# Kernel optimization log

Hardware: AMD Instinct MI355X
Metric: run time of the kernel (lower is better)

The kernel has to match this reference:

```python
import jax, jax.numpy as jnp
import numpy as np

NIN, DIM, NHEAD = 512, 64, 8
B, N = 2, 2048

def setup_inputs() -> dict:
    key = jax.random.key(0)
    ks = jax.random.split(key, 7)
    s = 1.0 / np.sqrt(NIN)  # torch Linear default init range
    out_f = DIM * NHEAD
    return {
        "x": jax.random.normal(ks[0], (B, N, NIN), dtype=jnp.float32),
        "Wq": jax.random.uniform(ks[1], (out_f, NIN), jnp.float32, -s, s),
        "bq": jax.random.uniform(ks[2], (out_f,), jnp.float32, -s, s),
        "Wk": jax.random.uniform(ks[3], (out_f, NIN), jnp.float32, -s, s),
        "bk": jax.random.uniform(ks[4], (out_f,), jnp.float32, -s, s),
        "Wv": jax.random.uniform(ks[5], (out_f, NIN), jnp.float32, -s, s),
        "bv": jax.random.uniform(ks[6], (out_f,), jnp.float32, -s, s),
    }

def reference(x, Wq, bq, Wk, bk, Wv, bv):
    b, n, nin = x.shape
    scale = DIM ** (-0.5)
    # torch: self.qs(x).view(nhead, B, N, dim) -- a FLAT reshape, not a transpose
    q = (x @ Wq.T + bq).reshape(NHEAD, b, n, DIM)
    k = (x @ Wk.T + bk).reshape(NHEAD, b, n, DIM)
    v = (x @ Wv.T + bv).reshape(NHEAD, b, n, DIM)
    # no softmax in the original module; mask path is a no-op (masked_fill not in-place)
    att = jnp.einsum('hbid,hbjd->hbij', q, k) * scale  # [h,b,n,n]
    out = jnp.einsum('hbij,hbjd->hbid', att, v)        # [h,b,n,d]
    out = jnp.transpose(out, (1, 2, 3, 0))             # [b,n,d,h]
    return out.reshape(b, n, -1)
```

## Files before the change

### kernel.cpp

```cpp
#include <hip/hip_runtime.h>
#include <stdint.h>

#define CHELEM 131072

typedef __attribute__((ext_vector_type(4))) float   f32x4;
typedef __attribute__((ext_vector_type(8))) short   bh8;
typedef __attribute__((ext_vector_type(4))) unsigned short u16x4;
typedef __attribute__((ext_vector_type(8))) unsigned short u16x8;
typedef unsigned short u16;

__device__ inline u16 f2bf(float f) {
    union { float f; uint32_t u; } v; v.f = f;
    uint32_t u = v.u;
    u += 0x7FFF + ((u >> 16) & 1);
    return (u16)(u >> 16);
}

__device__ inline void gload_lds16(const u16* g, u16* l) {
    __builtin_amdgcn_global_load_lds(
        (const __attribute__((address_space(1))) uint32_t*)g,
        (__attribute__((address_space(3)))       uint32_t*)l,
        16, 0, 0);
}

__global__ __launch_bounds__(256) void k0_convert(
        const float* __restrict__ x,
        const float* __restrict__ Wq,
        const float* __restrict__ Wk,
        const float* __restrict__ Wv,
        u16* __restrict__ xb, u16* __restrict__ Wb) {
    int idx = blockIdx.x * 256 + threadIdx.x;
    const float4* src; u16* dst; int off;
    if (idx < 524288) { src = (const float4*)x; dst = xb; off = idx; }
    else {
        int j = idx - 524288;
        int w = j >> 16;
        off = j & 65535;
        src = (const float4*)(w == 0 ? Wq : (w == 1 ? Wk : Wv));
        dst = Wb + w * 262144;
    }
    float4 f = src[off];
    u16x4 o;
    o[0] = f2bf(f.x); o[1] = f2bf(f.y); o[2] = f2bf(f.z); o[3] = f2bf(f.w);
    *(u16x4*)(dst + off * 4) = o;
}

__global__ __launch_bounds__(256) void k1_qkv(
        const u16* __restrict__ xb, const u16* __restrict__ Wb,
        const float* __restrict__ bq, const float* __restrict__ bk,
        const float* __restrict__ bv,
        u16* __restrict__ Qb, u16* __restrict__ Kb, u16* __restrict__ Vb) {
    __shared__ u16 smem[12288];
    u16* lA = smem;
    u16* lB = smem + 4096;
    const int tid  = threadIdx.x;
    const int lane = tid & 63, wid = tid >> 6;
    const int wr = wid >> 1, wc = wid & 1;
    const int swz  = (blockIdx.x & 7) * 96 + (blockIdx.x >> 3);
    const int mb = swz / 12, nb = swz % 12;
    const int w    = nb >> 2;
    const int nloc = (nb & 3) * 128;
    const u16*   W    = Wb + w * 262144;
    const float* bias = (w == 0) ? bq : ((w == 1) ? bk : bv);
    u16*         out  = (w == 0) ? Qb : ((w == 1) ? Kb : Vb);
    const int m0 = mb * 64;

    f32x4 acc[2][4] = {};
    const int srow = tid >> 3;
    const int scol = (tid & 7) * 8;

    for (int kb = 0; kb < 8; ++kb) {
        __syncthreads();
        const int k0 = kb * 64;
#pragma unroll
        for (int it = 0; it < 2; ++it) {
            int r = it * 32 + srow;
            gload_lds16(xb + (size_t)(m0 + r) * 512 + k0 + scol, lA + r * 64 + scol);
        }
#pragma unroll
        for (int it = 0; it < 4; ++it) {
            int r = it * 32 + srow;
            gload_lds16(W + (size_t)(nloc + r) * 512 + k0 + scol, lB + r * 64 + scol);
        }
        asm volatile("s_waitcnt vmcnt(0)" ::: "memory");
        __syncthreads();
#pragma unroll
        for (int ks = 0; ks < 2; ++ks) {
            const int kk = ks * 32 + (lane >> 4) * 8;
            bh8 a[2], b[4];
#pragma unroll
            for (int i = 0; i < 2; ++i)
                a[i] = *(const bh8*)&lA[(wr * 32 + i * 16 + (lane & 15)) * 64 + kk];
#pragma unroll
            for (int j = 0; j < 4; ++j)
                b[j] = *(const bh8*)&lB[(wc * 64 + j * 16 + (lane & 15)) * 64 + kk];
#pragma unroll
            for (int i = 0; i < 2; ++i)
#pragma unroll
                for (int j = 0; j < 4; ++j)
                    acc[i][j] = __builtin_amdgcn_mfma_f32_16x16x32_bf16(a[i], b[j], acc[i][j], 0, 0, 0);
        }
    }

    if (w == 0) {
#pragma unroll
        for (int i = 0; i < 2; ++i) {
            const int row_base = m0 + wr * 32 + i * 16 + ((lane >> 4) * 4);
#pragma unroll
            for (int j = 0; j < 4; ++j) {
                const int col = nloc + wc * 64 + j * 16 + (lane & 15);
                const float bv_ = bias[col];
#pragma unroll
                for (int r = 0; r < 4; ++r)
                    out[(size_t)(row_base + r) * 512 + col] = f2bf(acc[i][j][r] + bv_);
            }
        }
    } else {
        __syncthreads();
        u16 (*tile)[130] = (u16(*)[130])smem;
#pragma unroll
        for (int i = 0; i < 2; ++i) {
            const int ml = wr * 32 + i * 16 + ((lane >> 4) * 4);
#pragma unroll
            for (int j = 0; j < 4; ++j) {
                const int nl = wc * 64 + j * 16 + (lane & 15);
                const float bv_ = bias[nloc + nl];
#pragma unroll
                for (int r = 0; r < 4; ++r)
                    tile[ml + r][nl] = f2bf(acc[i][j][r] + bv_);
            }
        }
        __syncthreads();
        const int ncol  = tid & 127;
        const int mhalf = tid >> 7;
        const int g = (nb & 3) * 2 + (ncol >> 6);
        const int d = ncol & 63;
        const int c = mb >> 2;
        const int qbase = (mb & 3) * 64 + mhalf * 32;
        u16* dst = out + (size_t)c * CHELEM + d * 2048 + g * 256 + qbase;
#pragma unroll
        for (int v = 0; v < 4; ++v) {
            u16x8 t;
#pragma unroll
            for (int j = 0; j < 8; ++j)
                t[j] = tile[mhalf * 32 + v * 8 + j][ncol];
            *(u16x8*)(dst + v * 8) = t;
        }
    }
}

__global__ __launch_bounds__(256) void k2_pmat(
        const u16* __restrict__ Kt2, const u16* __restrict__ Vt2,
        u16* __restrict__ Pb) {
    __shared__ float red[4][16][16];
    const int tid = threadIdx.x;
    const int lane = tid & 63, w = tid >> 6;
    const int c   = blockIdx.x & 15;
    const int sub = blockIdx.x >> 4;
    const int dq = sub >> 2, eq = sub & 3;
    const u16* Vc = Vt2 + (size_t)c * CHELEM;
    const u16* Kc = Kt2 + (size_t)c * CHELEM;
    const int krow = lane & 15;
    const int arow = (dq * 16 + krow) * 2048;
    const int brow = (eq * 16 + krow) * 2048;
    const int kb = w * 512 + (lane >> 4) * 8;

    f32x4 acc = {};
#pragma unroll
    for (int kt = 0; kt < 16; ++kt) {
        const int k0 = kb + kt * 32;
        bh8 a = *(const bh8*)&Vc[arow + k0];
        bh8 b = *(const bh8*)&Kc[brow + k0];
        acc = __builtin_amdgcn_mfma_f32_16x16x32_bf16(a, b, acc, 0, 0, 0);
    }
#pragma unroll
    for (int r = 0; r < 4; ++r)
        red[w][(lane >> 4) * 4 + r][lane & 15] = acc[r];
    __syncthreads();
    const int row = tid >> 4, col = tid & 15;
    float s = red[0][row][col] + red[1][row][col] + red[2][row][col] + red[3][row][col];
    Pb[c * 4096 + (dq * 16 + row) * 64 + eq * 16 + col] = f2bf(s * 0.125f);
}

__global__ __launch_bounds__(256) void k3_out(
        const u16* __restrict__ Qb, const u16* __restrict__ Pb,
        float* __restrict__ outp) {
    const int tid = threadIdx.x;
    const int lane = tid & 63, w = tid >> 6;
    const int bb = blockIdx.x >> 6;
    const int ib = blockIdx.x & 63;
    const int i0 = ib * 32 + (w >> 1) * 16;
    const int dbase = (w & 1) * 32;
    const int krow = lane & 15;
    const int koff = (lane >> 4) * 8;

    f32x4 acc[8][2] = {};
#pragma unroll
    for (int h = 0; h < 8; ++h) {
        const int c = h * 2 + bb;
        const u16* Qc = Qb + (size_t)c * CHELEM;
        const u16* Pc = Pb + c * 4096;
#pragma unroll
        for (int ks = 0; ks < 2; ++ks) {
            bh8 a = *(const bh8*)&Qc[(i0 + krow) * 64 + ks * 32 + koff];
#pragma unroll
            for (int nf = 0; nf < 2; ++nf) {
                bh8 b = *(const bh8*)&Pc[(dbase + nf * 16 + krow) * 64 + ks * 32 + koff];
                acc[h][nf] = __builtin_amdgcn_mfma_f32_16x16x32_bf16(a, b, acc[h][nf], 0, 0, 0);
            }
        }
    }
    const int orow_base = bb * 2048 + ib * 32 + (w >> 1) * 16 + (lane >> 4) * 4;
#pragma unroll
    for (int nf = 0; nf < 2; ++nf) {
        const int d = dbase + nf * 16 + (lane & 15);
#pragma unroll
        for (int r = 0; r < 4; ++r) {
            f32x4 lo = {acc[0][nf][r], acc[1][nf][r], acc[2][nf][r], acc[3][nf][r]};
            f32x4 hi = {acc[4][nf][r], acc[5][nf][r], acc[6][nf][r], acc[7][nf][r]};
            float* dst = outp + (size_t)(orow_base + r) * 512 + d * 8;
            *(f32x4*)dst = lo;
            *(f32x4*)(dst + 4) = hi;
        }
    }
}

extern "C" void kernel_launch(void* const* d_in, const int* in_sizes, int n_in,
                              void* d_out, int out_size, void* d_ws, size_t ws_size,
                              hipStream_t stream) {
    const float* x  = (const float*)d_in[0];
    const float* Wq = (const float*)d_in[1];
    const float* bq = (const float*)d_in[2];
    const float* Wk = (const float*)d_in[3];
    const float* bk = (const float*)d_in[4];
    const float* Wv = (const float*)d_in[5];
    const float* bv = (const float*)d_in[6];
    float* outp = (float*)d_out;

    u16* xb = (u16*)d_ws;
    u16* Wb = xb + 2097152;
    u16* Qb = Wb + 786432;
    u16* Kb = Qb + 2097152;
    u16* Vb = Kb + 2097152;
    u16* Pb = Vb + 2097152;

    k0_convert<<<2816, 256, 0, stream>>>(x, Wq, Wk, Wv, xb, Wb);
    k1_qkv<<<768, 256, 0, stream>>>(xb, Wb, bq, bk, bv, Qb, Kb, Vb);
    k2_pmat<<<256, 256, 0, stream>>>(Kb, Vb, Pb);
    k3_out<<<128, 256, 0, stream>>>(Qb, Pb, outp);
}
```

Measured before the change: 41.20 us.

## Fuse P-matrix and output kernels with a global atomic flag barrier

Merges k2_pmat and k3_out into one 128-block launch. The first 16 blocks each compute a full 64x64 P matrix per chunk, using a 4x4 MFMA tile per wave and an LDS reduction across waves, then signal completion with an atomic counter. All blocks spin on that counter before running the Q·P output stage. This removes one kernel launch and its gap, but it relies on all 128 blocks being co-resident and puts all P work on only 16 blocks, which serialises that stage. The spin wait has an iteration cap, so it could time out and read P before it is written.

```diff
diff --git a/kernel.cpp b/kernel.cpp
--- a/kernel.cpp
+++ b/kernel.cpp
@@ -28,7 +28,10 @@
         const float* __restrict__ Wq,
         const float* __restrict__ Wk,
         const float* __restrict__ Wv,
-        u16* __restrict__ xb, u16* __restrict__ Wb) {
+        u16* __restrict__ xb, u16* __restrict__ Wb,
+        int* __restrict__ flag) {
+    if (blockIdx.x == 0 && threadIdx.x == 0)
+        __hip_atomic_store(flag, 0, __ATOMIC_RELAXED, __HIP_MEMORY_SCOPE_AGENT);
     int idx = blockIdx.x * 256 + threadIdx.x;
     const float4* src; u16* dst; int off;
     if (idx < 524288) { src = (const float4*)x; dst = xb; off = idx; }
@@ -149,52 +152,76 @@
     }
 }
 
-__global__ __launch_bounds__(256) void k2_pmat(
+__global__ __launch_bounds__(256) void k23_pv(
         const u16* __restrict__ Kt2, const u16* __restrict__ Vt2,
-        u16* __restrict__ Pb) {
-    __shared__ float red[4][16][16];
+        const u16* __restrict__ Qb, u16* __restrict__ Pb,
+        int* __restrict__ flag, float* __restrict__ outp) {
+    __shared__ float red[4][4096];
     const int tid = threadIdx.x;
     const int lane = tid & 63, w = tid >> 6;
-    const int c   = blockIdx.x & 15;
-    const int sub = blockIdx.x >> 4;
-    const int dq = sub >> 2, eq = sub & 3;
-    const u16* Vc = Vt2 + (size_t)c * CHELEM;
-    const u16* Kc = Kt2 + (size_t)c * CHELEM;
-    const int krow = lane & 15;
-    const int arow = (dq * 16 + krow) * 2048;
-    const int brow = (eq * 16 + krow) * 2048;
-    const int kb = w * 512 + (lane >> 4) * 8;
-
-    f32x4 acc = {};
-#pragma unroll
-    for (int kt = 0; kt < 16; ++kt) {
-        const int k0 = kb + kt * 32;
-        bh8 a = *(const bh8*)&Vc[arow + k0];
-        bh8 b = *(const bh8*)&Kc[brow + k0];
-        acc = __builtin_amdgcn_mfma_f32_16x16x32_bf16(a, b, acc, 0, 0, 0);
-    }
-#pragma unroll
-    for (int r = 0; r < 4; ++r)
-        red[w][(lane >> 4) * 4 + r][lane & 15] = acc[r];
+    const int bid = blockIdx.x;
+
+    if (bid < 16) {
+        const int c = bid;
+        const u16* Ac = Vt2 + (size_t)c * CHELEM;
+        const u16* Bc = Kt2 + (size_t)c * CHELEM;
+        f32x4 acc[4][4] = {};
+        const int krow = lane & 15;
+        const int kbase = w * 512 + (lane >> 4) * 8;
+#pragma unroll 4
+        for (int kt = 0; kt < 16; ++kt) {
+            const int k0 = kbase + kt * 32;
+            bh8 a[4], b[4];
+#pragma unroll
+            for (int i = 0; i < 4; ++i) {
+                a[i] = *(const bh8*)&Ac[(i * 16 + krow) * 2048 + k0];
+                b[i] = *(const bh8*)&Bc[(i * 16 + krow) * 2048 + k0];
+            }
+#pragma unroll
+            for (int i = 0; i < 4; ++i)
+#pragma unroll
+                for (int j = 0; j < 4; ++j)
+                    acc[i][j] = __builtin_amdgcn_mfma_f32_16x16x32_bf16(a[i], b[j], acc[i][j], 0, 0, 0);
+        }
+#pragma unroll
+        for (int i = 0; i < 4; ++i)
+#pragma unroll
+            for (int j = 0; j < 4; ++j)
+#pragma unroll
+                for (int r = 0; r < 4; ++r)
+                    red[w][(i * 16 + (lane >> 4) * 4 + r) * 64 + j * 16 + (lane & 15)] = acc[i][j][r];
+        __syncthreads();
+        u16* Pc = Pb + c * 4096;
+#pragma unroll
+        for (int q = 0; q < 16; ++q) {
+            const int idx = q * 256 + tid;
+            float s = red[0][idx] + red[1][idx] + red[2][idx] + red[3][idx];
+            Pc[idx] = f2bf(s * 0.125f);
+        }
+        __syncthreads();
+        if (tid == 0) {
+            __threadfence();
+            __hip_atomic_fetch_add(flag, 1, __ATOMIC_RELEASE, __HIP_MEMORY_SCOPE_AGENT);
+        }
+    }
+
+    if (tid == 0) {
+        int it = 0;
+        while (__hip_atomic_load(flag, __ATOMIC_ACQUIRE, __HIP_MEMORY_SCOPE_AGENT) < 16) {
+            __builtin_amdgcn_s_sleep(8);
+            if (++it > 1000000) break;
+        }
+    }
     __syncthreads();
-    const int row = tid >> 4, col = tid & 15;
-    float s = red[0][row][col] + red[1][row][col] + red[2][row][col] + red[3][row][col];
-    Pb[c * 4096 + (dq * 16 + row) * 64 + eq * 16 + col] = f2bf(s * 0.125f);
-}
-
-__global__ __launch_bounds__(256) void k3_out(
-        const u16* __restrict__ Qb, const u16* __restrict__ Pb,
-        float* __restrict__ outp) {
-    const int tid = threadIdx.x;
-    const int lane = tid & 63, w = tid >> 6;
-    const int bb = blockIdx.x >> 6;
-    const int ib = blockIdx.x & 63;
+
+    const int bb = bid >> 6;
+    const int ib = bid & 63;
     const int i0 = ib * 32 + (w >> 1) * 16;
     const int dbase = (w & 1) * 32;
     const int krow = lane & 15;
     const int koff = (lane >> 4) * 8;
 
-    f32x4 acc[8][2] = {};
+    f32x4 acc2[8][2] = {};
 #pragma unroll
     for (int h = 0; h < 8; ++h) {
         const int c = h * 2 + bb;
@@ -206,7 +233,7 @@
 #pragma unroll
             for (int nf = 0; nf < 2; ++nf) {
                 bh8 b = *(const bh8*)&Pc[(dbase + nf * 16 + krow) * 64 + ks * 32 + koff];
-                acc[h][nf] = __builtin_amdgcn_mfma_f32_16x16x32_bf16(a, b, acc[h][nf], 0, 0, 0);
+                acc2[h][nf] = __builtin_amdgcn_mfma_f32_16x16x32_bf16(a, b, acc2[h][nf], 0, 0, 0);
             }
         }
     }
@@ -216,8 +243,8 @@
         const int d = dbase + nf * 16 + (lane & 15);
 #pragma unroll
         for (int r = 0; r < 4; ++r) {
-            f32x4 lo = {acc[0][nf][r], acc[1][nf][r], acc[2][nf][r], acc[3][nf][r]};
-            f32x4 hi = {acc[4][nf][r], acc[5][nf][r], acc[6][nf][r], acc[7][nf][r]};
+            f32x4 lo = {acc2[0][nf][r], acc2[1][nf][r], acc2[2][nf][r], acc2[3][nf][r]};
+            f32x4 hi = {acc2[4][nf][r], acc2[5][nf][r], acc2[6][nf][r], acc2[7][nf][r]};
             float* dst = outp + (size_t)(orow_base + r) * 512 + d * 8;
             *(f32x4*)dst = lo;
             *(f32x4*)(dst + 4) = hi;
@@ -243,9 +270,9 @@
     u16* Kb = Qb + 2097152;
     u16* Vb = Kb + 2097152;
     u16* Pb = Vb + 2097152;
-
-    k0_convert<<<2816, 256, 0, stream>>>(x, Wq, Wk, Wv, xb, Wb);
+    int* flag = (int*)(Pb + 65536);
+
+    k0_convert<<<2816, 256, 0, stream>>>(x, Wq, Wk, Wv, xb, Wb, flag);
     k1_qkv<<<768, 256, 0, stream>>>(xb, Wb, bq, bk, bv, Qb, Kb, Vb);
-    k2_pmat<<<256, 256, 0, stream>>>(Kb, Vb, Pb);
-    k3_out<<<128, 256, 0, stream>>>(Qb, Pb, outp);
-}
+    k23_pv<<<128, 256, 0, stream>>>(Kb, Vb, Qb, Pb, flag, outp);
+}
```

Result: slower. 86.19 us (+109.2%).

## Fuse P-matrix and output kernels with a device-wide atomic barrier

Applied to the files above, without the earlier changes.

Merges the K^T V reduction kernel and the Q·P output kernel into one launch. An atomic counter acts as a grid-wide barrier: each block publishes its P tile, then spins until all 256 blocks have finished before starting the output GEMM. The output phase is re-tiled so each of the 256 blocks handles a 16-row slice. This removes one kernel launch and its gap, at the cost of relying on all 256 blocks being co-resident, plus a spin-wait with a timeout that could silently yield wrong results if the timeout is hit.

```diff
diff --git a/kernel.cpp b/kernel.cpp
--- a/kernel.cpp
+++ b/kernel.cpp
@@ -28,7 +28,10 @@
         const float* __restrict__ Wq,
         const float* __restrict__ Wk,
         const float* __restrict__ Wv,
-        u16* __restrict__ xb, u16* __restrict__ Wb) {
+        u16* __restrict__ xb, u16* __restrict__ Wb,
+        int* __restrict__ flag) {
+    if (blockIdx.x == 0 && threadIdx.x == 0)
+        __hip_atomic_store(flag, 0, __ATOMIC_RELAXED, __HIP_MEMORY_SCOPE_AGENT);
     int idx = blockIdx.x * 256 + threadIdx.x;
     const float4* src; u16* dst; int off;
     if (idx < 524288) { src = (const float4*)x; dst = xb; off = idx; }
@@ -149,52 +152,64 @@
     }
 }
 
-__global__ __launch_bounds__(256) void k2_pmat(
+__global__ __launch_bounds__(256) void k23_pv(
         const u16* __restrict__ Kt2, const u16* __restrict__ Vt2,
-        u16* __restrict__ Pb) {
+        const u16* __restrict__ Qb, u16* __restrict__ Pb,
+        int* __restrict__ flag, float* __restrict__ outp) {
     __shared__ float red[4][16][16];
     const int tid = threadIdx.x;
     const int lane = tid & 63, w = tid >> 6;
-    const int c   = blockIdx.x & 15;
-    const int sub = blockIdx.x >> 4;
-    const int dq = sub >> 2, eq = sub & 3;
-    const u16* Vc = Vt2 + (size_t)c * CHELEM;
-    const u16* Kc = Kt2 + (size_t)c * CHELEM;
-    const int krow = lane & 15;
-    const int arow = (dq * 16 + krow) * 2048;
-    const int brow = (eq * 16 + krow) * 2048;
-    const int kb = w * 512 + (lane >> 4) * 8;
-
-    f32x4 acc = {};
-#pragma unroll
-    for (int kt = 0; kt < 16; ++kt) {
-        const int k0 = kb + kt * 32;
-        bh8 a = *(const bh8*)&Vc[arow + k0];
-        bh8 b = *(const bh8*)&Kc[brow + k0];
-        acc = __builtin_amdgcn_mfma_f32_16x16x32_bf16(a, b, acc, 0, 0, 0);
-    }
-#pragma unroll
-    for (int r = 0; r < 4; ++r)
-        red[w][(lane >> 4) * 4 + r][lane & 15] = acc[r];
+    const int bid = blockIdx.x;
+
+    {
+        const int c   = bid & 15;
+        const int sub = bid >> 4;
+        const int dq = sub >> 2, eq = sub & 3;
+        const u16* Vc = Vt2 + (size_t)c * CHELEM;
+        const u16* Kc = Kt2 + (size_t)c * CHELEM;
+        const int krow = lane & 15;
+        const int arow = (dq * 16 + krow) * 2048;
+        const int brow = (eq * 16 + krow) * 2048;
+        const int kb = w * 512 + (lane >> 4) * 8;
+
+        f32x4 acc = {};
+#pragma unroll
+        for (int kt = 0; kt < 16; ++kt) {
+            const int k0 = kb + kt * 32;
+            bh8 a = *(const bh8*)&Vc[arow + k0];
+            bh8 b = *(const bh8*)&Kc[brow + k0];
+            acc = __builtin_amdgcn_mfma_f32_16x16x32_bf16(a, b, acc, 0, 0, 0);
+        }
+#pragma unroll
+        for (int r = 0; r < 4; ++r)
+            red[w][(lane >> 4) * 4 + r][lane & 15] = acc[r];
+        __syncthreads();
+        const int row = tid >> 4, col = tid & 15;
+        float s = red[0][row][col] + red[1][row][col] + red[2][row][col] + red[3][row][col];
+        Pb[c * 4096 + (dq * 16 + row) * 64 + eq * 16 + col] = f2bf(s * 0.125f);
+        __syncthreads();
+        if (tid == 0)
+            __hip_atomic_fetch_add(flag, 1, __ATOMIC_RELEASE, __HIP_MEMORY_SCOPE_AGENT);
+    }
+
+    if (tid == 0) {
+        int it = 0;
+        while (__hip_atomic_load(flag, __ATOMIC_RELAXED, __HIP_MEMORY_SCOPE_AGENT) < 256) {
+            __builtin_amdgcn_s_sleep(2);
+            if (++it > 200000) break;
+        }
+        (void)__hip_atomic_load(flag, __ATOMIC_ACQUIRE, __HIP_MEMORY_SCOPE_AGENT);
+    }
     __syncthreads();
-    const int row = tid >> 4, col = tid & 15;
-    float s = red[0][row][col] + red[1][row][col] + red[2][row][col] + red[3][row][col];
-    Pb[c * 4096 + (dq * 16 + row) * 64 + eq * 16 + col] = f2bf(s * 0.125f);
-}
-
-__global__ __launch_bounds__(256) void k3_out(
-        const u16* __restrict__ Qb, const u16* __restrict__ Pb,
-        float* __restrict__ outp) {
-    const int tid = threadIdx.x;
-    const int lane = tid & 63, w = tid >> 6;
-    const int bb = blockIdx.x >> 6;
-    const int ib = blockIdx.x & 63;
-    const int i0 = ib * 32 + (w >> 1) * 16;
-    const int dbase = (w & 1) * 32;
+
+    const int bb = bid >> 7;
+    const int ib = bid & 127;
+    const int i0 = ib * 16;
+    const int dbase = w * 16;
     const int krow = lane & 15;
     const int koff = (lane >> 4) * 8;
 
-    f32x4 acc[8][2] = {};
+    f32x4 acc2[8] = {};
 #pragma unroll
     for (int h = 0; h < 8; ++h) {
         const int c = h * 2 + bb;
@@ -203,25 +218,19 @@
 #pragma unroll
         for (int ks = 0; ks < 2; ++ks) {
             bh8 a = *(const bh8*)&Qc[(i0 + krow) * 64 + ks * 32 + koff];
-#pragma unroll
-            for (int nf = 0; nf < 2; ++nf) {
-                bh8 b = *(const bh8*)&Pc[(dbase + nf * 16 + krow) * 64 + ks * 32 + koff];
-                acc[h][nf] = __builtin_amdgcn_mfma_f32_16x16x32_bf16(a, b, acc[h][nf], 0, 0, 0);
-            }
-        }
-    }
-    const int orow_base = bb * 2048 + ib * 32 + (w >> 1) * 16 + (lane >> 4) * 4;
-#pragma unroll
-    for (int nf = 0; nf < 2; ++nf) {
-        const int d = dbase + nf * 16 + (lane & 15);
-#pragma unroll
-        for (int r = 0; r < 4; ++r) {
-            f32x4 lo = {acc[0][nf][r], acc[1][nf][r], acc[2][nf][r], acc[3][nf][r]};
-            f32x4 hi = {acc[4][nf][r], acc[5][nf][r], acc[6][nf][r], acc[7][nf][r]};
-            float* dst = outp + (size_t)(orow_base + r) * 512 + d * 8;
-            *(f32x4*)dst = lo;
-            *(f32x4*)(dst + 4) = hi;
-        }
+            bh8 b = *(const bh8*)&Pc[(dbase + krow) * 64 + ks * 32 + koff];
+            acc2[h] = __builtin_amdgcn_mfma_f32_16x16x32_bf16(a, b, acc2[h], 0, 0, 0);
+        }
+    }
+    const int orow_base = bb * 2048 + i0 + (lane >> 4) * 4;
+    const int d = dbase + (lane & 15);
+#pragma unroll
+    for (int r = 0; r < 4; ++r) {
+        f32x4 lo = {acc2[0][r], acc2[1][r], acc2[2][r], acc2[3][r]};
+        f32x4 hi = {acc2[4][r], acc2[5][r], acc2[6][r], acc2[7][r]};
+        float* dst = outp + (size_t)(orow_base + r) * 512 + d * 8;
+        *(f32x4*)dst = lo;
+        *(f32x4*)(dst + 4) = hi;
     }
 }
 
@@ -243,9 +252,9 @@
     u16* Kb = Qb + 2097152;
     u16* Vb = Kb + 2097152;
     u16* Pb = Vb + 2097152;
-
-    k0_convert<<<2816, 256, 0, stream>>>(x, Wq, Wk, Wv, xb, Wb);
+    int* flag = (int*)(Pb + 65536);
+
+    k0_convert<<<2816, 256, 0, stream>>>(x, Wq, Wk, Wv, xb, Wb, flag);
     k1_qkv<<<768, 256, 0, stream>>>(xb, Wb, bq, bk, bv, Qb, Kb, Vb);
-    k2_pmat<<<256, 256, 0, stream>>>(Kb, Vb, Pb);
-    k3_out<<<128, 256, 0, stream>>>(Qb, Pb, outp);
-}
+    k23_pv<<<256, 256, 0, stream>>>(Kb, Vb, Qb, Pb, flag, outp);
+}
```

New measurement: 46.51 us. 1.13x slower.
